# Performance work log

Hardware: AMD Instinct MI355X
Metric: run time of the kernel (lower is better)

## Reference

```python
import jax, jax.numpy as jnp
import numpy as np

B, Tr, P = 256, 512, 128
H, P_STD, P_STATIC, HEAD_H = 128, 32, 16, 64


def _uniform(key, shape, fan_in):
    bound = 1.0 / np.sqrt(fan_in)
    return jax.random.uniform(key, shape, jnp.float32, -bound, bound)


def setup_inputs() -> dict:
    key = jax.random.key(0)
    ks = jax.random.split(key, 16)
    X_raw = jax.random.normal(ks[0], (B, Tr, P), jnp.float32)
    M_raw = (jax.random.uniform(ks[1], (B, Tr, P)) < 0.7).astype(jnp.float32)
    DT_raw = jax.random.uniform(ks[2], (B, Tr, P), jnp.float32)
    STD_agg = jax.random.normal(ks[3], (B, 64, P_STD), jnp.float32)
    Z = jax.random.normal(ks[4], (B, P_STATIC), jnp.float32)
    idx_map = jax.random.randint(ks[5], (B, 64), -1, Tr)  # -1 marks invalid slots
    x_mean = jnp.zeros((P,), jnp.float32)  # non-trainable buffer-like param
    Wd = _uniform(ks[6], (H, P), P)
    bd = _uniform(ks[7], (H,), P)
    Wih = _uniform(ks[8], (3 * H, 2 * P), H)
    bih = _uniform(ks[9], (3 * H,), H)
    Whh = _uniform(ks[10], (3 * H, H), H)
    bhh = _uniform(ks[11], (3 * H,), H)
    W1 = _uniform(ks[12], (HEAD_H, H + P_STD + P_STATIC), H + P_STD + P_STATIC)
    b1 = _uniform(ks[13], (HEAD_H,), H + P_STD + P_STATIC)
    W2 = _uniform(ks[14], (1, HEAD_H), HEAD_H)
    return {"X_raw": X_raw, "M_raw": M_raw, "DT_raw": DT_raw, "STD_agg": STD_agg,
            "Z": Z, "idx_map": idx_map, "x_mean": x_mean, "Wd": Wd, "bd": bd,
            "Wih": Wih, "bih": bih, "Whh": Whh, "bhh": bhh,
            "W1": W1, "b1": b1, "W2": W2}


def reference(X_raw, M_raw, DT_raw, STD_agg, Z, idx_map, x_mean,
              Wd, bd, Wih, bih, Whh, bhh, W1, b1, W2):
    b, tr, p = X_raw.shape
    hdim = Whh.shape[1]

    def step(h, xs):
        x, m, dt = xs  # each [B, p]
        delta = jnp.exp(-jax.nn.softplus(dt))
        x_hat = m * x + (1 - m) * x_mean
        x_dec = m * x + (1 - m) * (delta * x_hat + (1 - delta) * x_mean)
        h_til = jnp.tanh(x_hat @ Wd.T + bd)
        h = delta * h + (1 - delta) * h_til  # requires p == hdim (as in source)
        inp = jnp.concatenate([x_dec, m], axis=-1)  # [B, 2p]
        gi = inp @ Wih.T + bih
        gh = h @ Whh.T + bhh
        gi_r, gi_z, gi_n = jnp.split(gi, 3, axis=-1)
        gh_r, gh_z, gh_n = jnp.split(gh, 3, axis=-1)
        r = jax.nn.sigmoid(gi_r + gh_r)
        z = jax.nn.sigmoid(gi_z + gh_z)
        n = jnp.tanh(gi_n + r * gh_n)
        h = (1 - z) * n + z * h
        return h, h

    h0 = jnp.zeros((b, hdim), X_raw.dtype)
    xs = (jnp.swapaxes(X_raw, 0, 1), jnp.swapaxes(M_raw, 0, 1), jnp.swapaxes(DT_raw, 0, 1))
    _, Hs = jax.lax.scan(step, h0, xs)  # [Tr, B, H]
    H_raw = jnp.swapaxes(Hs, 0, 1)  # [B, Tr, H]

    mask_sel = idx_map >= 0
    idx_safe = jnp.clip(idx_map, 0, None)
    H_agg = jnp.take_along_axis(H_raw, idx_safe[:, :, None], axis=1)
    H_agg = H_agg * mask_sel[:, :, None].astype(H_raw.dtype)  # [B, Ta, H]

    Ta = idx_map.shape[1]
    Zrep = jnp.broadcast_to(Z[:, None, :], (b, Ta, Z.shape[-1]))
    feats = jnp.concatenate([H_agg, STD_agg, Zrep], axis=-1)
    eta = (jax.nn.relu(feats @ W1.T + b1) @ W2.T)[..., 0]  # dropout is identity in eval
    return eta, H_raw, H_agg, mask_sel.astype(X_raw.dtype)
```

## Files before the change

### kernel.cpp

```cpp
#include <hip/hip_runtime.h>
#include <hip/hip_bf16.h>
#include <hip/hip_fp16.h>

#define B_    256
#define TR    512
#define P_    128
#define H_    128
#define NG    384
#define KI    256
#define TA    64
#define PSTD  32
#define PSTAT 16
#define HH    64
#define FDIM  176

#define TB    16
#define NT    (TR/TB)
#define TILE_BYTES 24576

typedef __attribute__((ext_vector_type(8))) short short8;
typedef __attribute__((ext_vector_type(4))) float f32x4;
typedef _Float16 f16;
typedef __attribute__((ext_vector_type(2))) _Float16 f16x2;

__device__ __forceinline__ float bf2f(ushort u) {
    union { uint i; float f; } v; v.i = ((uint)u) << 16; return v.f;
}
__device__ __forceinline__ ushort f2bf(float f) {
    union { float f; uint u; } v; v.f = f;
    uint u = v.u;
    uint r = (u + 0x7fffu + ((u >> 16) & 1u)) >> 16;
    return (ushort)r;
}
__device__ __forceinline__ float sigf(float x) {
    return 1.f / (1.f + __expf(-x));
}
__device__ __forceinline__ float tanhf_fast(float x) {
    float ax = fabsf(x);
    float e = __expf(-2.f * ax);
    float r = (1.f - e) / (1.f + e);
    return copysignf(r, x);
}
__device__ __forceinline__ void bar_lds() {
    __asm__ volatile("s_waitcnt lgkmcnt(0)\n\ts_barrier" ::: "memory");
}
__device__ __forceinline__ float dpp_add_xor1(float x) {
    int r = __builtin_amdgcn_mov_dpp(__float_as_int(x), 0xB1, 0xF, 0xF, true);
    return x + __int_as_float(r);
}
__device__ __forceinline__ float dpp_add_xor2(float x) {
    int r = __builtin_amdgcn_mov_dpp(__float_as_int(x), 0x4E, 0xF, 0xF, true);
    return x + __int_as_float(r);
}

__global__ __launch_bounds__(256) void k_convert(
    const float* __restrict__ Wih, const float* __restrict__ Wd,
    ushort* __restrict__ wih_b, ushort* __restrict__ wd_b)
{
    int i = blockIdx.x * 256 + threadIdx.x;
    if (i < NG * KI) wih_b[i] = f2bf(Wih[i]);
    if (i < H_ * P_) wd_b[i]  = f2bf(Wd[i]);
}

#define SA 392

__global__ __launch_bounds__(256, 2) void k_gemm(
    const float* __restrict__ X, const float* __restrict__ M,
    const float* __restrict__ DT, const float* __restrict__ xmean,
    const ushort* __restrict__ wih_b, const ushort* __restrict__ wd_b,
    const float* __restrict__ bih, const float* __restrict__ bd,
    ushort* __restrict__ gi_ws, ushort* __restrict__ htil_ws,
    float* __restrict__ delta_ws)
{
    __shared__ __align__(16) ushort sA[64 * SA];
    const int tid = threadIdx.x;
    const long r0 = (long)blockIdx.x * 64;

    #pragma unroll 4
    for (int i = 0; i < 32; ++i) {
        int idx = i * 256 + tid;
        int rl = idx >> 7, k = idx & 127;
        long g = (r0 + rl) * 128 + k;
        float x = X[g], m = M[g], dt = DT[g], xm = xmean[k];
        float delta = 1.f / (1.f + __expf(dt));
        float xh = m * x + (1.f - m) * xm;
        float xd = m * x + (1.f - m) * (delta * xh + (1.f - delta) * xm);
        sA[rl * SA + k]       = f2bf(xd);
        sA[rl * SA + 128 + k] = f2bf(m);
        sA[rl * SA + 256 + k] = f2bf(xh);
        delta_ws[g] = delta;
    }
    __syncthreads();

    const int wv   = tid >> 6;
    const int lane = tid & 63;
    const int l16  = lane & 15;
    const int q    = lane >> 4;

    f32x4 acc[4][6];
    #pragma unroll
    for (int rt = 0; rt < 4; ++rt)
        #pragma unroll
        for (int nt = 0; nt < 6; ++nt) acc[rt][nt] = (f32x4){0.f, 0.f, 0.f, 0.f};

    const int nb = 96 * wv;
    #pragma unroll
    for (int ks = 0; ks < 8; ++ks) {
        short8 a[4];
        #pragma unroll
        for (int rt = 0; rt < 4; ++rt)
            a[rt] = *(const short8*)&sA[(rt * 16 + l16) * SA + ks * 32 + q * 8];
        #pragma unroll
        for (int nt = 0; nt < 6; ++nt) {
            const short8 b = *(const short8*)&wih_b[(size_t)(nb + nt * 16 + l16) * KI + ks * 32 + q * 8];
            #pragma unroll
            for (int rt = 0; rt < 4; ++rt)
                acc[rt][nt] = __builtin_amdgcn_mfma_f32_16x16x32_bf16(a[rt], b, acc[rt][nt], 0, 0, 0);
        }
    }

    f32x4 acc2[4][2];
    #pragma unroll
    for (int rt = 0; rt < 4; ++rt)
        #pragma unroll
        for (int nt = 0; nt < 2; ++nt) acc2[rt][nt] = (f32x4){0.f, 0.f, 0.f, 0.f};

    const int nb2 = 32 * wv;
    #pragma unroll
    for (int ks = 0; ks < 4; ++ks) {
        short8 a[4];
        #pragma unroll
        for (int rt = 0; rt < 4; ++rt)
            a[rt] = *(const short8*)&sA[(rt * 16 + l16) * SA + 256 + ks * 32 + q * 8];
        #pragma unroll
        for (int nt = 0; nt < 2; ++nt) {
            const short8 b = *(const short8*)&wd_b[(size_t)(nb2 + nt * 16 + l16) * P_ + ks * 32 + q * 8];
            #pragma unroll
            for (int rt = 0; rt < 4; ++rt)
                acc2[rt][nt] = __builtin_amdgcn_mfma_f32_16x16x32_bf16(a[rt], b, acc2[rt][nt], 0, 0, 0);
        }
    }

    __syncthreads();

    ushort* sOut = sA;
    #pragma unroll
    for (int nt = 0; nt < 6; ++nt) {
        const int n = nb + nt * 16 + l16;
        const float bi = bih[n];
        #pragma unroll
        for (int rt = 0; rt < 4; ++rt) {
            #pragma unroll
            for (int reg = 0; reg < 4; ++reg) {
                int row = rt * 16 + q * 4 + reg;
                sOut[row * NG + n] = f2bf(acc[rt][nt][reg] + bi);
            }
        }
    }
    __syncthreads();

    {
        uint4* dst = (uint4*)(gi_ws + (size_t)r0 * NG);
        const uint4* src = (const uint4*)sOut;
        #pragma unroll
        for (int i = 0; i < 12; ++i) dst[tid + 256 * i] = src[tid + 256 * i];
    }
    __syncthreads();

    #pragma unroll
    for (int nt = 0; nt < 2; ++nt) {
        const int n = nb2 + nt * 16 + l16;
        const float bi = bd[n];
        #pragma unroll
        for (int rt = 0; rt < 4; ++rt) {
            #pragma unroll
            for (int reg = 0; reg < 4; ++reg) {
                int row = rt * 16 + q * 4 + reg;
                sOut[row * P_ + n] = f2bf(tanhf_fast(acc2[rt][nt][reg] + bi));
            }
        }
    }
    __syncthreads();

    {
        uint4* dst = (uint4*)(htil_ws + (size_t)r0 * P_);
        const uint4* src = (const uint4*)sOut;
        #pragma unroll
        for (int i = 0; i < 4; ++i) dst[tid + 256 * i] = src[tid + 256 * i];
    }
}

__global__ __launch_bounds__(512, 2) void k_scan(
    const ushort* __restrict__ gi_ws, const ushort* __restrict__ htil_ws,
    const float* __restrict__ delta_ws, const float* __restrict__ Whh,
    const float* __restrict__ bhh, float* __restrict__ Hraw)
{
    __shared__ __align__(16) char  s_in[2][TILE_BYTES];
    __shared__ __align__(16) float s_hout[TB * P_];
    __shared__ __align__(16) uint  s_hp16[2][80];

    const int tid = threadIdx.x;
    const int b   = blockIdx.x;
    const int j   = tid >> 2;
    const int q   = tid & 3;
    const long base = (long)b * TR;

    f16x2 wh[3][16];
    #pragma unroll
    for (int g = 0; g < 3; ++g) {
        const float* wp = Whh + ((g << 7) + j) * H_ + (q << 5);
        #pragma unroll
        for (int i = 0; i < 16; ++i) {
            f16x2 v;
            v[0] = (f16)wp[2 * i];
            v[1] = (f16)wp[2 * i + 1];
            wh[g][i] = v;
        }
    }
    float bh0 = 0.f, bh1 = 0.f, bh2 = 0.f;
    if (q == 0) { bh0 = bhh[j]; bh1 = bhh[128 + j]; bh2 = bhh[256 + j]; }

    {
        const uint4* gi4 = (const uint4*)(gi_ws   + (size_t)base * NG);
        const uint4* ht4 = (const uint4*)(htil_ws + (size_t)base * P_);
        const uint4* dl4 = (const uint4*)(delta_ws + (size_t)base * P_);
        uint4 p0 = gi4[tid];
        uint4 p1 = (tid < 256) ? gi4[512 + tid] : ht4[tid - 256];
        uint4 p2 = dl4[tid];
        uint4* d = (uint4*)s_in[0];
        d[tid] = p0; d[512 + tid] = p1; d[1024 + tid] = p2;
    }
    bar_lds();

    const int wpos = ((j >> 5) * 20 + ((j & 31) >> 1)) * 2 + (j & 1);

    int cur = 0, sb = 0;
    float h = 0.f, h_pre = 0.f;
    float d_c = 0.f, ht_c = 0.f, gr_c = 0.f, gz_c = 0.f, gn_c = 0.f;

    for (int tile = 0; tile < NT; ++tile) {
        uint4 p0, p1, p2;
        const int has_next = (tile + 1 < NT);
        if (has_next) {
            const long tn = base + (long)(tile + 1) * TB;
            const uint4* gi4 = (const uint4*)(gi_ws   + (size_t)tn * NG);
            const uint4* ht4 = (const uint4*)(htil_ws + (size_t)tn * P_);
            const uint4* dl4 = (const uint4*)(delta_ws + (size_t)tn * P_);
            p0 = gi4[tid];
            p1 = (tid < 256) ? gi4[512 + tid] : ht4[tid - 256];
            p2 = dl4[tid];
        }

        const ushort* sgi = (const ushort*)s_in[cur];
        const ushort* sht = (const ushort*)(s_in[cur] + 12288);
        const float*  sdl = (const float*) (s_in[cur] + 16384);

        if (q == 0) {
            d_c  = sdl[j];
            ht_c = bf2f(sht[j]);
            gr_c = bf2f(sgi[j]);
            gz_c = bf2f(sgi[128 + j]);
            gn_c = bf2f(sgi[256 + j]);
        }

        for (int ts = 0; ts < TB; ++ts) {
            if (q == 0) {
                h_pre = d_c * h + (1.f - d_c) * ht_c;
                ((f16*)s_hp16[sb])[wpos] = (f16)h_pre;
            }
            bar_lds();

            float d_n = d_c, ht_n = ht_c, gr_n = gr_c, gz_n = gz_c, gn_n = gn_c;
            if (q == 0 && ts + 1 < TB) {
                d_n  = sdl[(ts + 1) * P_ + j];
                ht_n = bf2f(sht[(ts + 1) * P_ + j]);
                gr_n = bf2f(sgi[(ts + 1) * NG + j]);
                gz_n = bf2f(sgi[(ts + 1) * NG + 128 + j]);
                gn_n = bf2f(sgi[(ts + 1) * NG + 256 + j]);
            }

            const uint4* hp = (const uint4*)&s_hp16[sb][q * 20];
            float ar0 = 0.f, ar1 = 0.f, az0 = 0.f, az1 = 0.f, an0 = 0.f, an1 = 0.f;
            #pragma unroll
            for (int i = 0; i < 4; ++i) {
                uint4 hv4 = hp[i];
                uint wds[4] = {hv4.x, hv4.y, hv4.z, hv4.w};
                #pragma unroll
                for (int k2 = 0; k2 < 4; ++k2) {
                    union { uint u; f16x2 h; } cv; cv.u = wds[k2];
                    const int ii = i * 4 + k2;
                    if (ii & 1) {
                        ar1 = __builtin_amdgcn_fdot2(cv.h, wh[0][ii], ar1, false);
                        az1 = __builtin_amdgcn_fdot2(cv.h, wh[1][ii], az1, false);
                        an1 = __builtin_amdgcn_fdot2(cv.h, wh[2][ii], an1, false);
                    } else {
                        ar0 = __builtin_amdgcn_fdot2(cv.h, wh[0][ii], ar0, false);
                        az0 = __builtin_amdgcn_fdot2(cv.h, wh[1][ii], az0, false);
                        an0 = __builtin_amdgcn_fdot2(cv.h, wh[2][ii], an0, false);
                    }
                }
            }
            float sr = ar0 + ar1, sz = az0 + az1, sn = an0 + an1;
            sr = dpp_add_xor2(dpp_add_xor1(sr));
            sz = dpp_add_xor2(dpp_add_xor1(sz));
            sn = dpp_add_xor2(dpp_add_xor1(sn));

            if (q == 0) {
                float r = sigf(gr_c + bh0 + sr);
                float z = sigf(gz_c + bh1 + sz);
                float n = tanhf_fast(gn_c + r * (bh2 + sn));
                h = (1.f - z) * n + z * h_pre;
                s_hout[ts * P_ + j] = h;
                d_c = d_n; ht_c = ht_n; gr_c = gr_n; gz_c = gz_n; gn_c = gn_n;
            }
            sb ^= 1;
        }

        bar_lds();

        {
            uint4* dst = (uint4*)(Hraw + (base + (long)tile * TB) * H_);
            dst[tid] = ((const uint4*)s_hout)[tid];
        }
        if (has_next) {
            uint4* d = (uint4*)s_in[cur ^ 1];
            d[tid] = p0; d[512 + tid] = p1; d[1024 + tid] = p2;
        }
        bar_lds();
        cur ^= 1;
    }
}

__global__ __launch_bounds__(256) void k_head(
    const float* __restrict__ Hraw, const float* __restrict__ STD,
    const float* __restrict__ Z, const int* __restrict__ idx_map,
    const float* __restrict__ W1, const float* __restrict__ b1,
    const float* __restrict__ W2,
    float* __restrict__ eta, float* __restrict__ Hagg,
    float* __restrict__ mask_out)
{
    __shared__ float sW1[HH * FDIM];
    __shared__ float sb1[HH], sW2[HH];
    __shared__ float spart[TA][4];

    const int tid = threadIdx.x, b = blockIdx.x;
    for (int i = tid; i < HH * FDIM; i += 256) sW1[i] = W1[i];
    if (tid < HH) { sb1[tid] = b1[tid]; sW2[tid] = W2[tid]; }
    __syncthreads();

    const int s = tid >> 2, p = tid & 3;
    const int idx = idx_map[b * TA + s];
    const int valid = idx >= 0;
    const int tt = valid ? idx : 0;
    const float* hrow = Hraw + ((long)b * TR + tt) * H_;

    float acc[16];
    #pragma unroll
    for (int uu = 0; uu < 16; ++uu) acc[uu] = sb1[p * 16 + uu];

    for (int f = 0; f < FDIM; ++f) {
        float feat;
        if (f < H_)              feat = valid ? hrow[f] : 0.f;
        else if (f < H_ + PSTD)  feat = STD[((long)b * TA + s) * PSTD + (f - H_)];
        else                     feat = Z[b * PSTAT + (f - H_ - PSTD)];
        #pragma unroll
        for (int uu = 0; uu < 16; ++uu)
            acc[uu] += feat * sW1[(p * 16 + uu) * FDIM + f];
    }

    float pe = 0.f;
    #pragma unroll
    for (int uu = 0; uu < 16; ++uu) {
        float a = acc[uu];
        pe += (a > 0.f ? a : 0.f) * sW2[p * 16 + uu];
    }
    spart[s][p] = pe;

    for (int e = 0; e < 32; ++e) {
        int ee = p * 32 + e;
        Hagg[((long)b * TA + s) * H_ + ee] = valid ? hrow[ee] : 0.f;
    }
    if (p == 0) mask_out[b * TA + s] = valid ? 1.f : 0.f;

    __syncthreads();
    if (tid < TA)
        eta[b * TA + tid] = spart[tid][0] + spart[tid][1] + spart[tid][2] + spart[tid][3];
}

extern "C" void kernel_launch(void* const* d_in, const int* in_sizes, int n_in,
                              void* d_out, int out_size, void* d_ws, size_t ws_size,
                              hipStream_t stream)
{
    const float* X     = (const float*)d_in[0];
    const float* M     = (const float*)d_in[1];
    const float* DT    = (const float*)d_in[2];
    const float* STD   = (const float*)d_in[3];
    const float* Z     = (const float*)d_in[4];
    const int*   idxm  = (const int*)  d_in[5];
    const float* xmean = (const float*)d_in[6];
    const float* Wd    = (const float*)d_in[7];
    const float* bd    = (const float*)d_in[8];
    const float* Wih   = (const float*)d_in[9];
    const float* bih   = (const float*)d_in[10];
    const float* Whh   = (const float*)d_in[11];
    const float* bhh   = (const float*)d_in[12];
    const float* W1    = (const float*)d_in[13];
    const float* b1    = (const float*)d_in[14];
    const float* W2    = (const float*)d_in[15];

    const long RROWS = (long)B_ * TR;
    char* ws = (char*)d_ws;
    size_t off = 0;
    ushort* gi_ws   = (ushort*)(ws + off); off += (size_t)RROWS * NG * 2;
    ushort* htil_ws = (ushort*)(ws + off); off += (size_t)RROWS * P_ * 2;
    float*  delta_ws= (float*) (ws + off); off += (size_t)RROWS * P_ * 4;
    ushort* wih_b   = (ushort*)(ws + off); off += (size_t)NG * KI * 2;
    ushort* wd_b    = (ushort*)(ws + off); off += (size_t)H_ * P_ * 2;

    float* out   = (float*)d_out;
    float* eta   = out;
    float* Hraw  = out + 16384;
    float* Hagg  = out + 16384 + (long)B_ * TR * H_;
    float* maskO = Hagg + (long)B_ * TA * H_;

    hipLaunchKernelGGL(k_convert, dim3(384), dim3(256), 0, stream,
                       Wih, Wd, wih_b, wd_b);
    hipLaunchKernelGGL(k_gemm, dim3(2048), dim3(256), 0, stream,
                       X, M, DT, xmean, wih_b, wd_b, bih, bd,
                       gi_ws, htil_ws, delta_ws);
    hipLaunchKernelGGL(k_scan, dim3(256), dim3(512), 0, stream,
                       gi_ws, htil_ws, delta_ws, Whh, bhh, Hraw);
    hipLaunchKernelGGL(k_head, dim3(256), dim3(256), 0, stream,
                       Hraw, STD, Z, idxm, W1, b1, W2, eta, Hagg, maskO);
}
```

Before: 740.4 us.

## Compute GRU gates redundantly in all lanes and write hidden state directly to global

In the recurrent scan kernel, all four lanes of each output group now compute the gate math, so the `q==0` divergence is gone. Only lane 0 stores h, and it writes straight to global memory instead of staging through shared memory, which also drops one barrier per tile. The sigmoid and tanh use the hardware reciprocal approximation, and the barrier helper is wrapped in scheduling barriers. The cost is redundant transcendental work per lane, narrow uncoalesced global stores, and slightly less accurate activations.

Measured after the change: 689.8 us. 1.07x faster.

```diff
diff --git a/kernel.cpp b/kernel.cpp
--- a/kernel.cpp
+++ b/kernel.cpp
@@ -41,8 +41,17 @@
     float r = (1.f - e) / (1.f + e);
     return copysignf(r, x);
 }
+__device__ __forceinline__ float sigf2(float x) {
+    return __builtin_amdgcn_rcpf(1.f + __expf(-x));
+}
+__device__ __forceinline__ float tanh2(float x) {
+    return 1.f - 2.f * __builtin_amdgcn_rcpf(1.f + __expf(2.f * x));
+}
 __device__ __forceinline__ void bar_lds() {
-    __asm__ volatile("s_waitcnt lgkmcnt(0)\n\ts_barrier" ::: "memory");
+    __builtin_amdgcn_sched_barrier(0);
+    __asm__ volatile("s_waitcnt lgkmcnt(0)");
+    __builtin_amdgcn_s_barrier();
+    __builtin_amdgcn_sched_barrier(0);
 }
 __device__ __forceinline__ float dpp_add_xor1(float x) {
     int r = __builtin_amdgcn_mov_dpp(__float_as_int(x), 0xB1, 0xF, 0xF, true);
@@ -196,7 +205,6 @@
     const float* __restrict__ bhh, float* __restrict__ Hraw)
 {
     __shared__ __align__(16) char  s_in[2][TILE_BYTES];
-    __shared__ __align__(16) float s_hout[TB * P_];
     __shared__ __align__(16) uint  s_hp16[2][80];
 
     const int tid = threadIdx.x;
@@ -217,8 +225,7 @@
             wh[g][i] = v;
         }
     }
-    float bh0 = 0.f, bh1 = 0.f, bh2 = 0.f;
-    if (q == 0) { bh0 = bhh[j]; bh1 = bhh[128 + j]; bh2 = bhh[256 + j]; }
+    const float bh0 = bhh[j], bh1 = bhh[128 + j], bh2 = bhh[256 + j];
 
     {
         const uint4* gi4 = (const uint4*)(gi_ws   + (size_t)base * NG);
@@ -235,8 +242,7 @@
     const int wpos = ((j >> 5) * 20 + ((j & 31) >> 1)) * 2 + (j & 1);
 
     int cur = 0, sb = 0;
-    float h = 0.f, h_pre = 0.f;
-    float d_c = 0.f, ht_c = 0.f, gr_c = 0.f, gz_c = 0.f, gn_c = 0.f;
+    float h = 0.f;
 
     for (int tile = 0; tile < NT; ++tile) {
         uint4 p0, p1, p2;
@@ -255,23 +261,20 @@
         const ushort* sht = (const ushort*)(s_in[cur] + 12288);
         const float*  sdl = (const float*) (s_in[cur] + 16384);
 
-        if (q == 0) {
-            d_c  = sdl[j];
-            ht_c = bf2f(sht[j]);
-            gr_c = bf2f(sgi[j]);
-            gz_c = bf2f(sgi[128 + j]);
-            gn_c = bf2f(sgi[256 + j]);
-        }
+        float d_c  = sdl[j];
+        float ht_c = bf2f(sht[j]);
+        float gr_c = bf2f(sgi[j]);
+        float gz_c = bf2f(sgi[128 + j]);
+        float gn_c = bf2f(sgi[256 + j]);
 
         for (int ts = 0; ts < TB; ++ts) {
-            if (q == 0) {
-                h_pre = d_c * h + (1.f - d_c) * ht_c;
+            float h_pre = d_c * h + (1.f - d_c) * ht_c;
+            if (q == 0)
                 ((f16*)s_hp16[sb])[wpos] = (f16)h_pre;
-            }
             bar_lds();
 
             float d_n = d_c, ht_n = ht_c, gr_n = gr_c, gz_n = gz_c, gn_n = gn_c;
-            if (q == 0 && ts + 1 < TB) {
+            if (ts + 1 < TB) {
                 d_n  = sdl[(ts + 1) * P_ + j];
                 ht_n = bf2f(sht[(ts + 1) * P_ + j]);
                 gr_n = bf2f(sgi[(ts + 1) * NG + j]);
@@ -305,29 +308,23 @@
             sz = dpp_add_xor2(dpp_add_xor1(sz));
             sn = dpp_add_xor2(dpp_add_xor1(sn));
 
-            if (q == 0) {
-                float r = sigf(gr_c + bh0 + sr);
-                float z = sigf(gz_c + bh1 + sz);
-                float n = tanhf_fast(gn_c + r * (bh2 + sn));
-                h = (1.f - z) * n + z * h_pre;
-                s_hout[ts * P_ + j] = h;
-                d_c = d_n; ht_c = ht_n; gr_c = gr_n; gz_c = gz_n; gn_c = gn_n;
-            }
+            float r = sigf2(gr_c + bh0 + sr);
+            float z = sigf2(gz_c + bh1 + sz);
+            float n = tanh2(gn_c + r * (bh2 + sn));
+            h = (1.f - z) * n + z * h_pre;
+            if (q == 0)
+                Hraw[(base + (long)tile * TB + ts) * P_ + j] = h;
+
+            d_c = d_n; ht_c = ht_n; gr_c = gr_n; gz_c = gz_n; gn_c = gn_n;
             sb ^= 1;
         }
 
-        bar_lds();
-
-        {
-            uint4* dst = (uint4*)(Hraw + (base + (long)tile * TB) * H_);
-            dst[tid] = ((const uint4*)s_hout)[tid];
-        }
         if (has_next) {
             uint4* d = (uint4*)s_in[cur ^ 1];
             d[tid] = p0; d[512 + tid] = p1; d[1024 + tid] = p2;
-        }
-        bar_lds();
-        cur ^= 1;
+            bar_lds();
+            cur ^= 1;
+        }
     }
 }
 
```
